# Kernel tuning notes

Hardware: AMD Instinct MI355X
Metric: run time of the kernel (lower is better)

The kernel has to match this reference:

```python
import jax, jax.numpy as jnp
import numpy as np

HEAD_DIM = 32
NUM_HEADS = 12
GP_NUM = 48
TOPK = 96


def setup_inputs() -> dict:
    key = jax.random.key(0)
    k0, k1, k2, k3 = jax.random.split(key, 4)
    B, H, W, C = 2, 40, 40, 384
    x = jax.random.normal(k0, (B, H, W, C), dtype=jnp.float32)
    w_qkv = jax.random.normal(k1, (3 * NUM_HEADS * HEAD_DIM, C), dtype=jnp.float32) * 0.05
    w_gp = jax.random.normal(k2, (GP_NUM, C), dtype=jnp.float32) * 0.05
    w_proj = jax.random.normal(k3, (C, NUM_HEADS * HEAD_DIM), dtype=jnp.float32) * 0.05
    return {"x": x, "w_qkv": w_qkv, "w_gp": w_gp, "w_proj": w_proj}


def _forward(x, w_qkv, w_gp, w_proj):
    B, H, W, C = x.shape
    N = H * W
    h, d, G, K = NUM_HEADS, HEAD_DIM, GP_NUM, TOPK
    scale = d ** -0.5
    qkv = (x.reshape(B, N, C) @ w_qkv.T).reshape(B, N, 3, h, d)
    qkv = qkv.transpose(2, 0, 3, 1, 4)  # [3,B,h,N,d]
    q, k, v = qkv[0], qkv[1], qkv[2]
    # dense attention [B,h,N,N]
    attn = jax.nn.softmax(jnp.einsum('bhnd,bhmd->bhnm', q, k) * scale, axis=-1)
    # query -> group routing (top-1 one-hot)
    gp = w_gp.reshape(h, G, d)
    group_logits = jnp.einsum('bhnd,hgd->bhng', q, gp)
    gidx = jnp.argmax(group_logits, axis=-1)  # [B,h,N]
    gw = jax.nn.one_hot(gidx, G, dtype=q.dtype)  # [B,h,N,G]
    # group-mean queries
    q_mean = jnp.einsum('bhng,bhnd->bhgd', gw, q)
    num_per_group = gw.sum(axis=2)[..., None]  # [B,h,G,1]
    q_mean = q_mean / jnp.clip(num_per_group, 1e-8)
    # group -> key routing (top-K scatter mask)
    qmw = jnp.einsum('bhgd,bhmd->bhgm', q_mean, k)  # [B,h,G,N]
    _, idx = jax.lax.top_k(qmw, K)  # [B,h,G,K]
    idx_flat = idx.reshape(-1, K)
    rows = jnp.arange(idx_flat.shape[0])[:, None]
    mask = jnp.zeros((idx_flat.shape[0], N), dtype=q.dtype).at[rows, idx_flat].set(1.0)
    mask = mask.reshape(qmw.shape)  # [B,h,G,N]
    # compose query->group and group->key masks, renormalize
    final = jnp.einsum('bhng,bhgm->bhnm', gw, mask)
    attn = attn * final
    attn = attn / jnp.clip(attn.sum(axis=-1, keepdims=True), 1e-8)
    out = jnp.einsum('bhnm,bhmd->bhnd', attn, v)
    out = out.transpose(0, 2, 1, 3).reshape(B, H, W, h * d)
    return out @ w_proj.T


def reference(x, w_qkv, w_gp, w_proj):
    return _forward(x, w_qkv, w_gp, w_proj)
```

## Files before the change

### kernel.cpp

```cpp
#include <hip/hip_runtime.h>
#include <math.h>

#define NH 12
#define HD 32
#define GN 48
#define TK 96
#define NB 2
#define NN 1600
#define CC 384
#define BHN (NB*NH)
#define QKV_COLS (3*NH*HD)
#define NQ (BHN*NN)

template<int MODE>
__global__ __launch_bounds__(256)
void gemm_tile(const float* __restrict__ A, const float* __restrict__ B,
               float* __restrict__ o0, float* __restrict__ o1, float* __restrict__ o2,
               int M, int N, int K)
{
    __shared__ float As[16][64];
    __shared__ float Bs[16][64];
    const int tid = threadIdx.x;
    const int tx = tid & 15, ty = tid >> 4;
    const int m0 = blockIdx.y * 64, n0 = blockIdx.x * 64;
    const int lr = tid >> 2;
    const int lc = (tid & 3) * 4;
    float acc[4][4] = {};

    for (int k0 = 0; k0 < K; k0 += 16) {
        float4 av = *(const float4*)&A[(m0 + lr) * K + k0 + lc];
        float4 bv = *(const float4*)&B[(n0 + lr) * K + k0 + lc];
        __syncthreads();
        As[lc+0][lr] = av.x; As[lc+1][lr] = av.y; As[lc+2][lr] = av.z; As[lc+3][lr] = av.w;
        Bs[lc+0][lr] = bv.x; Bs[lc+1][lr] = bv.y; Bs[lc+2][lr] = bv.z; Bs[lc+3][lr] = bv.w;
        __syncthreads();
        #pragma unroll
        for (int kk = 0; kk < 16; ++kk) {
            float4 a4 = *(const float4*)&As[kk][ty*4];
            float4 b4 = *(const float4*)&Bs[kk][tx*4];
            float a[4] = {a4.x, a4.y, a4.z, a4.w};
            float b[4] = {b4.x, b4.y, b4.z, b4.w};
            #pragma unroll
            for (int i = 0; i < 4; ++i)
                #pragma unroll
                for (int j = 0; j < 4; ++j)
                    acc[i][j] = fmaf(a[i], b[j], acc[i][j]);
        }
    }

    if (MODE == 0) {
        #pragma unroll
        for (int i = 0; i < 4; ++i) {
            int row = m0 + ty*4 + i;
            int b  = row / NN;
            int nn = row - b * NN;
            #pragma unroll
            for (int j = 0; j < 4; ++j) {
                int col = n0 + tx*4 + j;
                int which = col / CC;
                int rem = col - which * CC;
                int hh = rem >> 5, dd = rem & 31;
                float* dst = (which == 0) ? o0 : (which == 1) ? o1 : o2;
                dst[((b*NH + hh)*NN + nn)*HD + dd] = acc[i][j];
            }
        }
    } else {
        #pragma unroll
        for (int i = 0; i < 4; ++i) {
            int row = m0 + ty*4 + i;
            float4 st = make_float4(acc[i][0], acc[i][1], acc[i][2], acc[i][3]);
            *(float4*)&o0[row * N + n0 + tx*4] = st;
        }
    }
}

__global__ __launch_bounds__(256)
void group_route(const float* __restrict__ q, const float* __restrict__ wgp,
                 int* __restrict__ gidx)
{
    int t = blockIdx.x * 256 + threadIdx.x;
    int bh = t / NN;
    int hh = bh % NH;
    const float* qp = q + t * HD;
    float qr[HD];
    #pragma unroll
    for (int i = 0; i < HD; i += 4) {
        float4 x = *(const float4*)&qp[i];
        qr[i] = x.x; qr[i+1] = x.y; qr[i+2] = x.z; qr[i+3] = x.w;
    }
    float best = -INFINITY; int bg = 0;
    for (int g = 0; g < GN; ++g) {
        const float* gp = wgp + hh*GN*HD + g*HD;
        float s = 0.f;
        #pragma unroll
        for (int i = 0; i < HD; i += 4) {
            float4 w = *(const float4*)&gp[i];
            s += qr[i]*w.x + qr[i+1]*w.y + qr[i+2]*w.z + qr[i+3]*w.w;
        }
        if (s > best) { best = s; bg = g; }
    }
    gidx[t] = bg;
}

__global__ __launch_bounds__(256)
void qmean_all2(const float* __restrict__ q, const int* __restrict__ gidx,
                float* __restrict__ qmean)
{
    __shared__ float part[8][HD];
    __shared__ int   cnts[8];
    const int bid = blockIdx.x;
    const int g = bid % GN, bh = bid / GN;
    const int tid = threadIdx.x;
    const int s = tid >> 5, dd = tid & 31;

    const int* __restrict__ gx = gidx + bh*NN;
    const float* __restrict__ qb = q + bh*NN*HD;

    float p = 0.f; int c = 0;
    for (int n = s; n < NN; n += 8) {
        if (gx[n] == g) { p += qb[n*HD + dd]; c++; }
    }
    part[s][dd] = p;
    if (dd == 0) cnts[s] = c;
    __syncthreads();
    if (tid < HD) {
        float sum = 0.f; int ct = 0;
        #pragma unroll
        for (int ss = 0; ss < 8; ++ss) { sum += part[ss][tid]; ct += cnts[ss]; }
        qmean[bid*HD + tid] = ct ? sum / (float)ct : 0.f;
    }
}

__global__ __launch_bounds__(256)
void score_all(const float* __restrict__ qmean, const float* __restrict__ k,
               float* __restrict__ scores)
{
    __shared__ float Qs[GN][HD];
    const int bh = blockIdx.y;
    const int tid = threadIdx.x;
    const int n = blockIdx.x*256 + tid;
    for (int i = tid; i < GN*HD; i += 256)
        ((float*)Qs)[i] = qmean[bh*GN*HD + i];
    __syncthreads();
    if (n >= NN) return;
    const float* __restrict__ kp = k + (bh*NN + n)*HD;
    float4 kr[8];
    #pragma unroll
    for (int c = 0; c < 8; ++c) kr[c] = *(const float4*)&kp[c*4];
    for (int g = 0; g < GN; ++g) {
        float s = 0.f;
        #pragma unroll
        for (int c = 0; c < 8; ++c) {
            float4 qv = *(const float4*)&Qs[g][c*4];
            s += kr[c].x*qv.x + kr[c].y*qv.y + kr[c].z*qv.z + kr[c].w*qv.w;
        }
        scores[(bh*GN + g)*NN + n] = s;
    }
}

__global__ __launch_bounds__(256)
void topk_radix(const float* __restrict__ scores, int* __restrict__ topk)
{
    __shared__ unsigned keysL[4][NN];
    __shared__ unsigned histL[4][256];
    const int tid = threadIdx.x;
    const int w = tid >> 6, lane = tid & 63;
    const int gid = blockIdx.x*4 + w;
    const float* __restrict__ row = scores + gid*NN;
    unsigned* keys = keysL[w];
    unsigned* hist = histL[w];

    #pragma unroll
    for (int i = 0; i < 25; ++i) {
        int m = lane + 64*i;
        unsigned u = __float_as_uint(row[m]);
        u = (u & 0x80000000u) ? ~u : (u | 0x80000000u);
        keys[m] = u;
    }

    unsigned prefix = 0, r = TK;
    #pragma unroll
    for (int pass = 0; pass < 4; ++pass) {
        const int shift = 24 - 8*pass;
        #pragma unroll
        for (int j = 0; j < 4; ++j) hist[lane*4 + j] = 0;
        #pragma unroll
        for (int i = 0; i < 25; ++i) {
            unsigned u = keys[lane + 64*i];
            bool match = (pass == 0) || ((u >> (shift+8)) == (prefix >> (shift+8)));
            if (match) atomicAdd(&hist[(u >> shift) & 255u], 1u);
        }
        uint4 h = *(const uint4*)&hist[lane*4];
        unsigned s3 = h.w, s2 = h.z + s3, s1 = h.y + s2, s0 = h.x + s1;
        unsigned I = s0;
        #pragma unroll
        for (int off = 1; off < 64; off <<= 1) {
            unsigned t = __shfl_down(I, off);
            if (lane + off < 64) I += t;
        }
        unsigned E = I - s0;
        unsigned sf[5] = {E+s0, E+s1, E+s2, E+s3, E};
        int bj = -1; unsigned subc = 0;
        #pragma unroll
        for (int j = 0; j < 4; ++j)
            if (sf[j] >= r && sf[j+1] < r) { bj = j; subc = sf[j+1]; }
        unsigned long long mask = __ballot(bj >= 0);
        int src = __ffsll(mask) - 1;
        int bstar = __shfl(lane*4 + bj, src);
        unsigned sub = (unsigned)__shfl((int)subc, src);
        prefix |= ((unsigned)bstar) << shift;
        r -= sub;
    }
    const unsigned P = prefix;

    int* tko = topk + gid*TK;
    int base = 0;
    #pragma unroll
    for (int i = 0; i < 25; ++i) {
        int m = lane + 64*i;
        bool gt = (keys[m] > P);
        unsigned long long mask = __ballot(gt);
        if (gt) tko[base + __popcll(mask & ((1ull << lane) - 1ull))] = m;
        base += (int)__popcll(mask);
    }
    #pragma unroll
    for (int i = 0; i < 25; ++i) {
        int m = lane + 64*i;
        bool eq = (keys[m] == P);
        unsigned long long mask = __ballot(eq);
        if (eq) {
            int pos = base + (int)__popcll(mask & ((1ull << lane) - 1ull));
            if (pos < TK) tko[pos] = m;
        }
        base += (int)__popcll(mask);
    }
}

__global__ __launch_bounds__(256)
void sparse_attn4(const float* __restrict__ q, const float* __restrict__ k,
                  const float* __restrict__ v, const int* __restrict__ gidx,
                  const int* __restrict__ topk, float* __restrict__ out)
{
    const float scale = 0.17677669529663687f;
    const int tid = threadIdx.x;
    const int qs = tid >> 3;
    const int dl = tid & 7;
    const int Q  = blockIdx.x * 32 + qs;
    const int bh = Q / NN, nn = Q - bh * NN;
    const int lb = (tid & 63) & ~7;

    const int g = gidx[Q];
    const int* __restrict__ tk = topk + (bh*GN + g) * TK;
    const float* __restrict__ kb = k + bh * NN * HD;
    const float* __restrict__ vb = v + bh * NN * HD;

    float4 q4 = *(const float4*)&q[Q * HD + dl*4];

    int ki[12];
    #pragma unroll
    for (int t = 0; t < 12; ++t) ki[t] = tk[t*8 + dl];

    float sc[12];
    #pragma unroll
    for (int t = 0; t < 12; ++t) {
        float keep = 0.f;
        #pragma unroll
        for (int u = 0; u < 8; ++u) {
            int kj = __shfl(ki[t], lb + u);
            float4 w = *(const float4*)&kb[kj*HD + dl*4];
            float p = fmaf(q4.x, w.x, fmaf(q4.y, w.y, fmaf(q4.z, w.z, q4.w*w.w)));
            p += __shfl_xor(p, 1);
            p += __shfl_xor(p, 2);
            p += __shfl_xor(p, 4);
            if (u == dl) keep = p;
        }
        sc[t] = keep * scale;
    }

    float m = -INFINITY;
    #pragma unroll
    for (int t = 0; t < 12; ++t) m = fmaxf(m, sc[t]);
    #pragma unroll
    for (int off = 1; off < 8; off <<= 1) m = fmaxf(m, __shfl_xor(m, off));
    float l = 0.f;
    #pragma unroll
    for (int t = 0; t < 12; ++t) { sc[t] = __expf(sc[t] - m); l += sc[t]; }
    #pragma unroll
    for (int off = 1; off < 8; off <<= 1) l += __shfl_xor(l, off);
    float inv = 1.0f / l;
    #pragma unroll
    for (int t = 0; t < 12; ++t) sc[t] *= inv;

    float a0 = 0.f, a1 = 0.f, a2 = 0.f, a3 = 0.f;
    #pragma unroll
    for (int t = 0; t < 12; ++t) {
        #pragma unroll
        for (int jj = 0; jj < 8; ++jj) {
            int   kj = __shfl(ki[t], lb + jj);
            float p  = __shfl(sc[t], lb + jj);
            float4 vv = *(const float4*)&vb[kj*HD + dl*4];
            a0 = fmaf(p, vv.x, a0);
            a1 = fmaf(p, vv.y, a1);
            a2 = fmaf(p, vv.z, a2);
            a3 = fmaf(p, vv.w, a3);
        }
    }

    const int b = bh / NH, hh = bh - b*NH;
    float* op = out + (b*NN + nn)*CC + hh*HD + dl*4;
    *(float4*)op = make_float4(a0, a1, a2, a3);
}

extern "C" void kernel_launch(void* const* d_in, const int* in_sizes, int n_in,
                              void* d_out, int out_size, void* d_ws, size_t ws_size,
                              hipStream_t stream)
{
    const float* x      = (const float*)d_in[0];
    const float* w_qkv  = (const float*)d_in[1];
    const float* w_gp   = (const float*)d_in[2];
    const float* w_proj = (const float*)d_in[3];
    float* out = (float*)d_out;

    float* ws = (float*)d_ws;
    float* q        = ws;
    float* kk       = ws + 1228800;
    float* vv       = ws + 2457600;
    float* attn_out = ws + 3686400;
    float* scores   = ws + 4915200;
    float* qmean    = ws + 6758400;
    int*   iws      = (int*)(ws + 6795264);
    int*   gidx     = iws;
    int*   topk     = iws + 38400;

    gemm_tile<0><<<dim3(QKV_COLS/64, (NB*NN)/64), 256, 0, stream>>>(
        x, w_qkv, q, kk, vv, NB*NN, QKV_COLS, CC);

    group_route<<<NQ/256, 256, 0, stream>>>(q, w_gp, gidx);

    qmean_all2<<<BHN*GN, 256, 0, stream>>>(q, gidx, qmean);

    score_all<<<dim3(7, BHN), 256, 0, stream>>>(qmean, kk, scores);

    topk_radix<<<(BHN*GN)/4, 256, 0, stream>>>(scores, topk);

    sparse_attn4<<<NQ/32, 256, 0, stream>>>(q, kk, vv, gidx, topk, attn_out);

    gemm_tile<1><<<dim3(CC/64, (NB*NN)/64), 256, 0, stream>>>(
        attn_out, w_proj, out, nullptr, nullptr, NB*NN, CC, CC);
}
```

Baseline: 298.6 us.

## Group queries by routed group and stage shared top-K keys/values in LDS

The qmean kernel now also builds a per-group permutation of query indices, with offsets and counts. The sparse attention kernel is relaunched with one block per (batch, head, group). Each block loads that group's 96 selected K and V rows into shared memory once, then loops over all queries routed to that group. This replaces the per-query gathered global loads of K/V with shared-memory reuse. The cost is load imbalance, since group sizes vary and empty groups return early, plus extra atomics and passes in the qmean kernel.

```diff
diff --git a/kernel.cpp b/kernel.cpp
--- a/kernel.cpp
+++ b/kernel.cpp
@@ -104,10 +104,12 @@
 
 __global__ __launch_bounds__(256)
 void qmean_all2(const float* __restrict__ q, const int* __restrict__ gidx,
-                float* __restrict__ qmean)
+                float* __restrict__ qmean, int* __restrict__ qperm,
+                int* __restrict__ qoff, int* __restrict__ qcnt)
 {
     __shared__ float part[8][HD];
     __shared__ int   cnts[8];
+    __shared__ int   off_s, pos_s;
     const int bid = blockIdx.x;
     const int g = bid % GN, bh = bid / GN;
     const int tid = threadIdx.x;
@@ -115,6 +117,8 @@
 
     const int* __restrict__ gx = gidx + bh*NN;
     const float* __restrict__ qb = q + bh*NN*HD;
+
+    if (tid == 0) { off_s = 0; pos_s = 0; }
 
     float p = 0.f; int c = 0;
     for (int n = s; n < NN; n += 8) {
@@ -123,12 +127,26 @@
     part[s][dd] = p;
     if (dd == 0) cnts[s] = c;
     __syncthreads();
+
     if (tid < HD) {
         float sum = 0.f; int ct = 0;
         #pragma unroll
         for (int ss = 0; ss < 8; ++ss) { sum += part[ss][tid]; ct += cnts[ss]; }
         qmean[bid*HD + tid] = ct ? sum / (float)ct : 0.f;
     }
+
+    int mo = 0;
+    for (int n = tid; n < NN; n += 256) mo += (gx[n] < g);
+    atomicAdd(&off_s, mo);
+    __syncthreads();
+    for (int n = tid; n < NN; n += 256) {
+        if (gx[n] == g) {
+            int pp = atomicAdd(&pos_s, 1);
+            qperm[bh*NN + off_s + pp] = n;
+        }
+    }
+    __syncthreads();
+    if (tid == 0) { qoff[bid] = off_s; qcnt[bid] = pos_s; }
 }
 
 __global__ __launch_bounds__(256)
@@ -236,79 +254,98 @@
     }
 }
 
-__global__ __launch_bounds__(256)
-void sparse_attn4(const float* __restrict__ q, const float* __restrict__ k,
-                  const float* __restrict__ v, const int* __restrict__ gidx,
-                  const int* __restrict__ topk, float* __restrict__ out)
-{
+__global__ __launch_bounds__(256, 4)
+void sparse_attn5(const float* __restrict__ q, const float* __restrict__ k,
+                  const float* __restrict__ v, const int* __restrict__ topk,
+                  const int* __restrict__ qperm, const int* __restrict__ qoff,
+                  const int* __restrict__ qcnt, float* __restrict__ out)
+{
+    __shared__ float Ks[TK*HD];
+    __shared__ float Vs[TK*HD];
+
+    const int bid = blockIdx.x;
+    const int bh = bid / GN;
+    const int nq = qcnt[bid];
+    if (nq == 0) return;
+    const int off = qoff[bid];
+    const int tid = threadIdx.x;
+
+    const int* __restrict__ tk = topk + bid*TK;
+    const float* __restrict__ kb = k + bh*NN*HD;
+    const float* __restrict__ vb = v + bh*NN*HD;
+
+    for (int idx = tid; idx < TK*8; idx += 256) {
+        int row = idx >> 3, ch = idx & 7;
+        int r = tk[row];
+        ((float4*)Ks)[idx] = *(const float4*)&kb[r*HD + ch*4];
+        ((float4*)Vs)[idx] = *(const float4*)&vb[r*HD + ch*4];
+    }
+    __syncthreads();
+
     const float scale = 0.17677669529663687f;
-    const int tid = threadIdx.x;
     const int qs = tid >> 3;
     const int dl = tid & 7;
-    const int Q  = blockIdx.x * 32 + qs;
-    const int bh = Q / NN, nn = Q - bh * NN;
     const int lb = (tid & 63) & ~7;
-
-    const int g = gidx[Q];
-    const int* __restrict__ tk = topk + (bh*GN + g) * TK;
-    const float* __restrict__ kb = k + bh * NN * HD;
-    const float* __restrict__ vb = v + bh * NN * HD;
-
-    float4 q4 = *(const float4*)&q[Q * HD + dl*4];
-
-    int ki[12];
-    #pragma unroll
-    for (int t = 0; t < 12; ++t) ki[t] = tk[t*8 + dl];
-
-    float sc[12];
-    #pragma unroll
-    for (int t = 0; t < 12; ++t) {
-        float keep = 0.f;
-        #pragma unroll
-        for (int u = 0; u < 8; ++u) {
-            int kj = __shfl(ki[t], lb + u);
-            float4 w = *(const float4*)&kb[kj*HD + dl*4];
-            float p = fmaf(q4.x, w.x, fmaf(q4.y, w.y, fmaf(q4.z, w.z, q4.w*w.w)));
-            p += __shfl_xor(p, 1);
-            p += __shfl_xor(p, 2);
-            p += __shfl_xor(p, 4);
-            if (u == dl) keep = p;
-        }
-        sc[t] = keep * scale;
-    }
-
-    float m = -INFINITY;
-    #pragma unroll
-    for (int t = 0; t < 12; ++t) m = fmaxf(m, sc[t]);
-    #pragma unroll
-    for (int off = 1; off < 8; off <<= 1) m = fmaxf(m, __shfl_xor(m, off));
-    float l = 0.f;
-    #pragma unroll
-    for (int t = 0; t < 12; ++t) { sc[t] = __expf(sc[t] - m); l += sc[t]; }
-    #pragma unroll
-    for (int off = 1; off < 8; off <<= 1) l += __shfl_xor(l, off);
-    float inv = 1.0f / l;
-    #pragma unroll
-    for (int t = 0; t < 12; ++t) sc[t] *= inv;
-
-    float a0 = 0.f, a1 = 0.f, a2 = 0.f, a3 = 0.f;
-    #pragma unroll
-    for (int t = 0; t < 12; ++t) {
-        #pragma unroll
-        for (int jj = 0; jj < 8; ++jj) {
-            int   kj = __shfl(ki[t], lb + jj);
-            float p  = __shfl(sc[t], lb + jj);
-            float4 vv = *(const float4*)&vb[kj*HD + dl*4];
-            a0 = fmaf(p, vv.x, a0);
-            a1 = fmaf(p, vv.y, a1);
-            a2 = fmaf(p, vv.z, a2);
-            a3 = fmaf(p, vv.w, a3);
-        }
-    }
-
     const int b = bh / NH, hh = bh - b*NH;
-    float* op = out + (b*NN + nn)*CC + hh*HD + dl*4;
-    *(float4*)op = make_float4(a0, a1, a2, a3);
+    const float* __restrict__ qbase = q + bh*NN*HD;
+    const int* __restrict__ qlist = qperm + bh*NN + off;
+
+    for (int it0 = 0; it0 < nq; it0 += 32) {
+        const int qi = it0 + qs;
+        const bool act = (qi < nq);
+        const int nn = qlist[act ? qi : nq-1];
+
+        float4 q4 = *(const float4*)&qbase[nn*HD + dl*4];
+
+        float sc[12];
+        #pragma unroll
+        for (int t = 0; t < 12; ++t) {
+            float keep = 0.f;
+            #pragma unroll
+            for (int u = 0; u < 8; ++u) {
+                float4 w = *(const float4*)&Ks[(t*8 + u)*HD + dl*4];
+                float p = fmaf(q4.x, w.x, fmaf(q4.y, w.y, fmaf(q4.z, w.z, q4.w*w.w)));
+                p += __shfl_xor(p, 1);
+                p += __shfl_xor(p, 2);
+                p += __shfl_xor(p, 4);
+                if (u == dl) keep = p;
+            }
+            sc[t] = keep * scale;
+        }
+
+        float m = -INFINITY;
+        #pragma unroll
+        for (int t = 0; t < 12; ++t) m = fmaxf(m, sc[t]);
+        #pragma unroll
+        for (int o = 1; o < 8; o <<= 1) m = fmaxf(m, __shfl_xor(m, o));
+        float l = 0.f;
+        #pragma unroll
+        for (int t = 0; t < 12; ++t) { sc[t] = __expf(sc[t] - m); l += sc[t]; }
+        #pragma unroll
+        for (int o = 1; o < 8; o <<= 1) l += __shfl_xor(l, o);
+        const float inv = 1.0f / l;
+        #pragma unroll
+        for (int t = 0; t < 12; ++t) sc[t] *= inv;
+
+        float a0 = 0.f, a1 = 0.f, a2 = 0.f, a3 = 0.f;
+        #pragma unroll
+        for (int t = 0; t < 12; ++t) {
+            #pragma unroll
+            for (int u = 0; u < 8; ++u) {
+                const float p = __shfl(sc[t], lb + u);
+                float4 vv = *(const float4*)&Vs[(t*8 + u)*HD + dl*4];
+                a0 = fmaf(p, vv.x, a0);
+                a1 = fmaf(p, vv.y, a1);
+                a2 = fmaf(p, vv.z, a2);
+                a3 = fmaf(p, vv.w, a3);
+            }
+        }
+
+        if (act) {
+            float* op = out + (b*NN + nn)*CC + hh*HD + dl*4;
+            *(float4*)op = make_float4(a0, a1, a2, a3);
+        }
+    }
 }
 
 extern "C" void kernel_launch(void* const* d_in, const int* in_sizes, int n_in,
@@ -331,19 +368,22 @@
     int*   iws      = (int*)(ws + 6795264);
     int*   gidx     = iws;
     int*   topk     = iws + 38400;
+    int*   qperm    = iws + 38400 + 110592;
+    int*   qoff     = iws + 38400 + 110592 + 38400;
+    int*   qcnt     = qoff + 1152;
 
     gemm_tile<0><<<dim3(QKV_COLS/64, (NB*NN)/64), 256, 0, stream>>>(
         x, w_qkv, q, kk, vv, NB*NN, QKV_COLS, CC);
 
     group_route<<<NQ/256, 256, 0, stream>>>(q, w_gp, gidx);
 
-    qmean_all2<<<BHN*GN, 256, 0, stream>>>(q, gidx, qmean);
+    qmean_all2<<<BHN*GN, 256, 0, stream>>>(q, gidx, qmean, qperm, qoff, qcnt);
 
     score_all<<<dim3(7, BHN), 256, 0, stream>>>(qmean, kk, scores);
 
     topk_radix<<<(BHN*GN)/4, 256, 0, stream>>>(scores, topk);
 
-    sparse_attn4<<<NQ/32, 256, 0, stream>>>(q, kk, vv, gidx, topk, attn_out);
+    sparse_attn5<<<BHN*GN, 256, 0, stream>>>(q, kk, vv, topk, qperm, qoff, qcnt, attn_out);
 
     gemm_tile<1><<<dim3(CC/64, (NB*NN)/64), 256, 0, stream>>>(
         attn_out, w_proj, out, nullptr, nullptr, NB*NN, CC, CC);
```

Result: slower. 585.6 us (+96.1%).
